# Performance work log

Measured on AMD Instinct MI355X. Metric: run time of the kernel, lower is better.

Reference implementation:

```python
import jax, jax.numpy as jnp
import numpy as np

TOP_K = 2

def setup_inputs() -> dict:
    key = jax.random.key(0)
    k0, k1, k2, k3 = jax.random.split(key, 4)
    B, T, D, F, E = 2, 2048, 1024, 4096, 8
    x = jax.random.normal(k0, (B, T, D), dtype=jnp.float32)
    Wr = jax.random.normal(k1, (E, D), dtype=jnp.float32) * 0.02   # router weight [out=E, in=D]
    W1 = jax.random.normal(k2, (E, F, D), dtype=jnp.float32) * 0.02  # per-expert up-proj [out=F, in=D]
    W2 = jax.random.normal(k3, (E, D, F), dtype=jnp.float32) * 0.02  # per-expert down-proj [out=D, in=F]
    return {"x": x, "Wr": Wr, "W1": W1, "W2": W2}

def reference(x, Wr, W1, W2):
    B, T, D = x.shape
    E = Wr.shape[0]
    N = B * T
    xf = x.reshape(N, D)
    # Router in fp32 on the un-cast activations (as in the torch module).
    logits = xf @ Wr.T                                   # [N, E]
    probs = jax.nn.softmax(logits, axis=-1)
    topk_w, topk_idx = jax.lax.top_k(probs, TOP_K)       # [N, K]
    topk_w = topk_w / jnp.sum(topk_w, axis=-1, keepdims=True)
    # Combine weights scattered into a dense [N, E] dispatch/combine matrix
    # (top_k indices are distinct, so .set is exact).
    combine = jnp.zeros((N, E), dtype=jnp.float32)
    combine = combine.at[jnp.arange(N)[:, None], topk_idx].set(topk_w)
    # Expert FFN runs in bf16 (comm_dtype in the original all-to-all pipeline).
    xb = xf.astype(jnp.bfloat16)
    h = jax.nn.gelu(jnp.einsum('nd,efd->enf', xb, W1.astype(jnp.bfloat16)),
                    approximate=False)                   # [E, N, F]
    yo = jnp.einsum('enf,edf->end', h, W2.astype(jnp.bfloat16))  # [E, N, D]
    # Weighted combine: bf16 expert outputs * fp32 gate weights -> fp32 (torch promotion).
    out = jnp.einsum('end,ne->nd', yo.astype(jnp.float32), combine)
    return out.reshape(B, T, D)
```

## Files before the change

kernel.cpp:

```cpp
#include <hip/hip_runtime.h>
#include <hip/hip_bf16.h>

typedef __attribute__((ext_vector_type(8))) __bf16 bf16x8;
typedef __attribute__((ext_vector_type(4))) float floatx4;

constexpr int N_TOK = 4096;
constexpr int DDIM  = 1024;
constexpr int FDIM  = 4096;
constexpr int NEXP  = 8;
constexpr int NSLOT = 2 * N_TOK;
constexpr int BM_T  = 256;
constexpr int MAXT  = NSLOT / BM_T + NEXP - 1;
constexpr int KSPLIT = 2;

static __device__ __forceinline__ unsigned short f2bf(float f) {
    union { __hip_bfloat16 h; unsigned short u; } v;
    v.h = __float2bfloat16(f);
    return v.u;
}

static __device__ __forceinline__ void gl2lds16(const unsigned short* g, unsigned short* l) {
    __builtin_amdgcn_global_load_lds(
        (__attribute__((address_space(1))) void*)g,
        (__attribute__((address_space(3))) void*)l,
        16, 0, 0);
}

__global__ void castW_kernel(const float* __restrict__ W1, const float* __restrict__ W2,
                             unsigned short* __restrict__ w1b, unsigned short* __restrict__ w2b,
                             int* __restrict__ counts) {
    constexpr int HALF = NEXP * FDIM * DDIM / 4;
    int i = blockIdx.x * 256 + threadIdx.x;
    const float* s; unsigned short* d; int j;
    if (i < HALF) { s = W1; d = w1b; j = i; }
    else          { s = W2; d = w2b; j = i - HALF; }
    float4 v = *(const float4*)(s + (size_t)j * 4);
    ushort4 o;
    o.x = f2bf(v.x); o.y = f2bf(v.y); o.z = f2bf(v.z); o.w = f2bf(v.w);
    *(ushort4*)(d + (size_t)j * 4) = o;
    if (blockIdx.x == 0 && threadIdx.x < NEXP) counts[threadIdx.x] = 0;
}

__global__ void router_kernel(const float* __restrict__ x, const float* __restrict__ Wr,
                              unsigned short* __restrict__ xb,
                              int* __restrict__ te, float* __restrict__ tw,
                              int* __restrict__ counts) {
    __shared__ float wr[NEXP * DDIM];
    const int tid = threadIdx.x;
    for (int i = tid; i < NEXP * DDIM; i += 256) wr[i] = Wr[i];
    __syncthreads();
    const int wave = tid >> 6, lane = tid & 63;
    const int t = blockIdx.x * 4 + wave;

    float xr[16];
    const float* xp = x + (size_t)t * DDIM;
    #pragma unroll
    for (int i = 0; i < 16; i++) xr[i] = xp[lane + 64 * i];

    unsigned short* xbp = xb + (size_t)t * DDIM;
    #pragma unroll
    for (int i = 0; i < 16; i++) xbp[lane + 64 * i] = f2bf(xr[i]);

    float logit[NEXP];
    #pragma unroll
    for (int e = 0; e < NEXP; e++) {
        float s = 0.f;
        #pragma unroll
        for (int i = 0; i < 16; i++) s += xr[i] * wr[e * DDIM + lane + 64 * i];
        #pragma unroll
        for (int off = 32; off > 0; off >>= 1) s += __shfl_xor(s, off, 64);
        logit[e] = s;
    }
    if (lane == 0) {
        int i0 = 0; float l0 = logit[0];
        #pragma unroll
        for (int e = 1; e < NEXP; e++) if (logit[e] > l0) { l0 = logit[e]; i0 = e; }
        int i1 = -1; float l1 = -3.0e38f;
        #pragma unroll
        for (int e = 0; e < NEXP; e++) if (e != i0 && logit[e] > l1) { l1 = logit[e]; i1 = e; }
        float p1 = expf(l1 - l0);
        float w0 = 1.f / (1.f + p1);
        float w1 = p1 * w0;
        te[t * 2] = i0; te[t * 2 + 1] = i1;
        tw[t * 2] = w0; tw[t * 2 + 1] = w1;
        atomicAdd(&counts[i0], 1);
        atomicAdd(&counts[i1], 1);
    }
}

__global__ void scan_scatter_kernel(const int* __restrict__ counts,
                                    const int* __restrict__ te, const float* __restrict__ tw,
                                    int* __restrict__ offsets, int* __restrict__ tile_em,
                                    int* __restrict__ ntile,
                                    int* __restrict__ rowid, float* __restrict__ gate,
                                    int* __restrict__ tok2slot) {
    __shared__ int soff[NEXP];
    __shared__ int scur[NEXP];
    const int tid = threadIdx.x;
    if (tid == 0) {
        int acc = 0, nt = 0;
        for (int e = 0; e < NEXP; e++) {
            offsets[e] = acc; soff[e] = acc;
            for (int m0 = 0; m0 < counts[e]; m0 += BM_T)
                tile_em[nt++] = (e << 16) | (m0 >> 8);
            acc += counts[e];
        }
        offsets[NEXP] = acc;
        ntile[0] = nt;
        for (int i = nt; i < MAXT; i++) tile_em[i] = 0;
    }
    if (tid < NEXP) scur[tid] = 0;
    __syncthreads();
    for (int t = tid; t < N_TOK; t += 256) {
        #pragma unroll
        for (int k = 0; k < 2; k++) {
            int e = te[t * 2 + k];
            int pos = atomicAdd(&scur[e], 1);
            int slot = soff[e] + pos;
            rowid[slot] = t;
            gate[slot] = tw[t * 2 + k];
            tok2slot[t * 2 + k] = slot;
        }
    }
}

template <bool UP>
__global__ __launch_bounds__(512, 4)
void ffn_gemm(const unsigned short* __restrict__ A,
              const unsigned short* __restrict__ Wb,
              unsigned short* __restrict__ Hout,
              float* __restrict__ Y,
              const int* __restrict__ rowid,
              const float* __restrict__ gate,
              const int* __restrict__ offsets,
              const int* __restrict__ tile_em,
              const int* __restrict__ ntile) {
    constexpr int BM = 256, BN = 128, BK = 32;
    constexpr int NOUT = UP ? FDIM : DDIM;
    constexpr int KDIM = UP ? DDIM : FDIM;
    constexpr int NN   = NOUT / BN;
    constexpr int KLEN = UP ? DDIM : (FDIM / KSPLIT);
    constexpr int KT   = KLEN / BK;
    constexpr int MREP = 4, NREP = 4;
    constexpr int ASTRIDE = BM * BK;
    constexpr int BSTRIDE = BN * BK;

    const int nwg = NN * MAXT * (UP ? 1 : KSPLIT);
    const int orig = blockIdx.x;
    const int xcd = orig & 7, idx = orig >> 3;
    const int qq = nwg >> 3, rr8 = nwg & 7;
    const int id = (xcd < rr8 ? xcd * (qq + 1) : rr8 * (qq + 1) + (xcd - rr8) * qq) + idx;

    const int n0 = (id % NN) * BN;
    const int bt = (id / NN) % MAXT;
    const int ks = UP ? 0 : (id / (NN * MAXT));
    if (bt >= ntile[0]) return;
    const int em = tile_em[bt];
    const int e  = em >> 16;
    const int m0 = (em & 0xffff) << 8;
    const int seg = offsets[e];
    const int cnt = offsets[e + 1] - seg;
    const int kbase = ks * KLEN;

    __shared__ __align__(16) unsigned short As[2 * ASTRIDE];
    __shared__ __align__(16) unsigned short Bs[2 * BSTRIDE];

    const int tid  = threadIdx.x;
    const int lane = tid & 63;
    const int wave = tid >> 6;
    const int lrow = lane >> 2;
    const int chunk = lane & 3;
    const int scol = (chunk ^ (lrow & 3)) * 8;

    const unsigned short* ag[2];
    #pragma unroll
    for (int j = 0; j < 2; j++) {
        int arow = wave * 32 + j * 16 + lrow;
        int slot = seg + m0 + arow;
        if (slot >= NSLOT) slot = NSLOT - 1;
        if (UP) { int t = rowid[slot]; ag[j] = A + (size_t)t * DDIM + kbase + scol; }
        else    { ag[j] = A + (size_t)slot * FDIM + kbase + scol; }
    }
    const unsigned short* bg0 =
        Wb + ((size_t)e * NOUT + n0 + wave * 16 + lrow) * KDIM + kbase + scol;

    unsigned short* asl[2];
    #pragma unroll
    for (int j = 0; j < 2; j++)
        asl[j] = &As[(wave * 32 + j * 16) * BK] + lane * 8;
    unsigned short* bsl0 = &Bs[(wave * 16) * BK] + lane * 8;

    auto stage = [&](int b) {
        gl2lds16(ag[0], asl[0] + b * ASTRIDE); ag[0] += BK;
        gl2lds16(ag[1], asl[1] + b * ASTRIDE); ag[1] += BK;
        gl2lds16(bg0,   bsl0   + b * BSTRIDE); bg0   += BK;
    };

    const int frow = lane & 15;
    const int quad = lane >> 4;
    const int wm = (wave >> 1) * 64;
    const int wn = (wave & 1) * 64;
    const int cs = ((quad ^ (frow & 3)) * 8);

    floatx4 acc[MREP][NREP];
    #pragma unroll
    for (int i = 0; i < MREP; i++)
        #pragma unroll
        for (int j = 0; j < NREP; j++)
            acc[i][j] = (floatx4){0.f, 0.f, 0.f, 0.f};

    stage(0);
    __syncthreads();
    for (int kt = 0; kt < KT; kt++) {
        if (kt + 1 < KT) stage((kt + 1) & 1);
        const unsigned short* Ab = &As[(kt & 1) * ASTRIDE];
        const unsigned short* Bb = &Bs[(kt & 1) * BSTRIDE];
        bf16x8 av[MREP], bv[NREP];
        #pragma unroll
        for (int i = 0; i < MREP; i++)
            av[i] = *(const bf16x8*)&Ab[(wm + i * 16 + frow) * BK + cs];
        #pragma unroll
        for (int j = 0; j < NREP; j++)
            bv[j] = *(const bf16x8*)&Bb[(wn + j * 16 + frow) * BK + cs];
        #pragma unroll
        for (int i = 0; i < MREP; i++)
            #pragma unroll
            for (int j = 0; j < NREP; j++)
                acc[i][j] = __builtin_amdgcn_mfma_f32_16x16x32_bf16(av[i], bv[j], acc[i][j], 0, 0, 0);
        __syncthreads();
    }

    #pragma unroll
    for (int mt = 0; mt < MREP; mt++) {
        #pragma unroll
        for (int rg = 0; rg < 4; rg++) {
            int mloc = m0 + wm + mt * 16 + quad * 4 + rg;
            if (mloc >= cnt) continue;
            int slot = seg + mloc;
            if (UP) {
                #pragma unroll
                for (int nt = 0; nt < NREP; nt++) {
                    int n = n0 + wn + nt * 16 + frow;
                    float v = acc[mt][nt][rg];
                    float g = 0.5f * v * (1.0f + erff(v * 0.70710678118654752f));
                    Hout[(size_t)slot * FDIM + n] = f2bf(g);
                }
            } else {
                float gw = gate[slot];
                #pragma unroll
                for (int nt = 0; nt < NREP; nt++) {
                    int n = n0 + wn + nt * 16 + frow;
                    Y[((size_t)ks * NSLOT + slot) * DDIM + n] = gw * acc[mt][nt][rg];
                }
            }
        }
    }
}

__global__ void combine_kernel(const float* __restrict__ Y, const int* __restrict__ tok2slot,
                               float* __restrict__ out) {
    int idx = blockIdx.x * 256 + threadIdx.x;
    int t = idx >> 8;
    int c = (idx & 255) * 4;
    int s0 = tok2slot[t * 2], s1 = tok2slot[t * 2 + 1];
    float4 r = make_float4(0.f, 0.f, 0.f, 0.f);
    #pragma unroll
    for (int ks = 0; ks < KSPLIT; ks++) {
        float4 a = *(const float4*)(Y + ((size_t)ks * NSLOT + s0) * DDIM + c);
        float4 b = *(const float4*)(Y + ((size_t)ks * NSLOT + s1) * DDIM + c);
        r.x += a.x + b.x; r.y += a.y + b.y; r.z += a.z + b.z; r.w += a.w + b.w;
    }
    *(float4*)(out + (size_t)t * DDIM + c) = r;
}

extern "C" void kernel_launch(void* const* d_in, const int* in_sizes, int n_in,
                              void* d_out, int out_size, void* d_ws, size_t ws_size,
                              hipStream_t stream) {
    const float* x  = (const float*)d_in[0];
    const float* Wr = (const float*)d_in[1];
    const float* W1 = (const float*)d_in[2];
    const float* W2 = (const float*)d_in[3];
    float* out = (float*)d_out;

    char* ws = (char*)d_ws;
    size_t off = 0;
    auto alloc = [&](size_t bytes) -> char* {
        char* p = ws + off;
        off = (off + bytes + 255) & ~(size_t)255;
        return p;
    };
    unsigned short* xb   = (unsigned short*)alloc((size_t)N_TOK * DDIM * 2);
    unsigned short* H    = (unsigned short*)alloc((size_t)NSLOT * FDIM * 2);
    float* Yb      = (float*)alloc((size_t)KSPLIT * NSLOT * DDIM * 4);
    int*   rowid   = (int*)alloc(NSLOT * 4);
    float* gatew   = (float*)alloc(NSLOT * 4);
    int*   te      = (int*)alloc(NSLOT * 4);
    float* tw      = (float*)alloc(NSLOT * 4);
    int*   t2s     = (int*)alloc(NSLOT * 4);
    int*   counts  = (int*)alloc(64);
    int*   offsets = (int*)alloc(64);
    int*   tile_em = (int*)alloc(MAXT * 4);
    int*   ntile   = (int*)alloc(64);
    unsigned short* w1b = (unsigned short*)alloc((size_t)NEXP * FDIM * DDIM * 2);
    unsigned short* w2b = (unsigned short*)alloc((size_t)NEXP * DDIM * FDIM * 2);
    (void)ws_size;

    constexpr int GRID_UP = (FDIM / 128) * MAXT;
    constexpr int GRID_DN = (DDIM / 128) * MAXT * KSPLIT;

    castW_kernel<<<2 * NEXP * FDIM * DDIM / 4 / 256, 256, 0, stream>>>(W1, W2, w1b, w2b, counts);
    router_kernel<<<N_TOK / 4, 256, 0, stream>>>(x, Wr, xb, te, tw, counts);
    scan_scatter_kernel<<<1, 256, 0, stream>>>(counts, te, tw, offsets, tile_em, ntile,
                                               rowid, gatew, t2s);
    ffn_gemm<true ><<<GRID_UP, 512, 0, stream>>>(xb, w1b, H, Yb, rowid, gatew,
                                                 offsets, tile_em, ntile);
    ffn_gemm<false><<<GRID_DN, 512, 0, stream>>>(H, w2b, H, Yb, rowid, gatew,
                                                 offsets, tile_em, ntile);
    combine_kernel<<<N_TOK, 256, 0, stream>>>(Yb, t2s, out);
}
```

Baseline: 683.9 us.

## Shrink GEMM tiles to 128x128 with 256 threads and triple-buffered LDS pipeline

Changes the expert FFN GEMMs from 256x128 tiles with 512 threads to 128x128 tiles with 256 threads. This halves the per-tile row granularity, which cuts padding waste on each expert's last tile and produces more workgroups. The K loop moves to a three-stage LDS ring with explicit vmcnt waits and raw barriers, so two loads stay in flight, and MFMA sections get raised wave priority. The LDS swizzle also changes to reduce bank conflicts. In exchange there is less reuse per tile, more B-weight traffic per output, and hand-written waitcnt logic that could be fragile.

Result: faster. 664.3 us (-2.9%).

```diff
diff --git a/kernel.cpp b/kernel.cpp
--- a/kernel.cpp
+++ b/kernel.cpp
@@ -9,7 +9,7 @@
 constexpr int FDIM  = 4096;
 constexpr int NEXP  = 8;
 constexpr int NSLOT = 2 * N_TOK;
-constexpr int BM_T  = 256;
+constexpr int BM_T  = 128;
 constexpr int MAXT  = NSLOT / BM_T + NEXP - 1;
 constexpr int KSPLIT = 2;
 
@@ -102,7 +102,7 @@
         for (int e = 0; e < NEXP; e++) {
             offsets[e] = acc; soff[e] = acc;
             for (int m0 = 0; m0 < counts[e]; m0 += BM_T)
-                tile_em[nt++] = (e << 16) | (m0 >> 8);
+                tile_em[nt++] = (e << 16) | (m0 >> 7);
             acc += counts[e];
         }
         offsets[NEXP] = acc;
@@ -125,7 +125,7 @@
 }
 
 template <bool UP>
-__global__ __launch_bounds__(512, 4)
+__global__ __launch_bounds__(256, 3)
 void ffn_gemm(const unsigned short* __restrict__ A,
               const unsigned short* __restrict__ Wb,
               unsigned short* __restrict__ Hout,
@@ -135,7 +135,7 @@
               const int* __restrict__ offsets,
               const int* __restrict__ tile_em,
               const int* __restrict__ ntile) {
-    constexpr int BM = 256, BN = 128, BK = 32;
+    constexpr int BM = 128, BN = 128, BK = 32;
     constexpr int NOUT = UP ? FDIM : DDIM;
     constexpr int KDIM = UP ? DDIM : FDIM;
     constexpr int NN   = NOUT / BN;
@@ -157,20 +157,20 @@
     if (bt >= ntile[0]) return;
     const int em = tile_em[bt];
     const int e  = em >> 16;
-    const int m0 = (em & 0xffff) << 8;
+    const int m0 = (em & 0xffff) << 7;
     const int seg = offsets[e];
     const int cnt = offsets[e + 1] - seg;
     const int kbase = ks * KLEN;
 
-    __shared__ __align__(16) unsigned short As[2 * ASTRIDE];
-    __shared__ __align__(16) unsigned short Bs[2 * BSTRIDE];
+    __shared__ __align__(16) unsigned short As[3 * ASTRIDE];
+    __shared__ __align__(16) unsigned short Bs[3 * BSTRIDE];
 
     const int tid  = threadIdx.x;
     const int lane = tid & 63;
     const int wave = tid >> 6;
     const int lrow = lane >> 2;
     const int chunk = lane & 3;
-    const int scol = (chunk ^ (lrow & 3)) * 8;
+    const int scol = (chunk ^ ((lrow >> 1) & 3)) * 8;
 
     const unsigned short* ag[2];
     #pragma unroll
@@ -181,26 +181,32 @@
         if (UP) { int t = rowid[slot]; ag[j] = A + (size_t)t * DDIM + kbase + scol; }
         else    { ag[j] = A + (size_t)slot * FDIM + kbase + scol; }
     }
-    const unsigned short* bg0 =
-        Wb + ((size_t)e * NOUT + n0 + wave * 16 + lrow) * KDIM + kbase + scol;
-
+    const unsigned short* bg[2];
+    #pragma unroll
+    for (int j = 0; j < 2; j++) {
+        int brow = wave * 32 + j * 16 + lrow;
+        bg[j] = Wb + ((size_t)e * NOUT + n0 + brow) * KDIM + kbase + scol;
+    }
     unsigned short* asl[2];
-    #pragma unroll
-    for (int j = 0; j < 2; j++)
+    unsigned short* bsl[2];
+    #pragma unroll
+    for (int j = 0; j < 2; j++) {
         asl[j] = &As[(wave * 32 + j * 16) * BK] + lane * 8;
-    unsigned short* bsl0 = &Bs[(wave * 16) * BK] + lane * 8;
+        bsl[j] = &Bs[(wave * 32 + j * 16) * BK] + lane * 8;
+    }
 
     auto stage = [&](int b) {
         gl2lds16(ag[0], asl[0] + b * ASTRIDE); ag[0] += BK;
         gl2lds16(ag[1], asl[1] + b * ASTRIDE); ag[1] += BK;
-        gl2lds16(bg0,   bsl0   + b * BSTRIDE); bg0   += BK;
+        gl2lds16(bg[0], bsl[0] + b * BSTRIDE); bg[0] += BK;
+        gl2lds16(bg[1], bsl[1] + b * BSTRIDE); bg[1] += BK;
     };
 
     const int frow = lane & 15;
     const int quad = lane >> 4;
     const int wm = (wave >> 1) * 64;
     const int wn = (wave & 1) * 64;
-    const int cs = ((quad ^ (frow & 3)) * 8);
+    const int cs = (quad ^ ((frow >> 1) & 3)) * 8;
 
     floatx4 acc[MREP][NREP];
     #pragma unroll
@@ -210,11 +216,17 @@
             acc[i][j] = (floatx4){0.f, 0.f, 0.f, 0.f};
 
     stage(0);
-    __syncthreads();
-    for (int kt = 0; kt < KT; kt++) {
-        if (kt + 1 < KT) stage((kt + 1) & 1);
-        const unsigned short* Ab = &As[(kt & 1) * ASTRIDE];
-        const unsigned short* Bb = &Bs[(kt & 1) * BSTRIDE];
+    stage(1);
+    asm volatile("s_waitcnt vmcnt(4)" ::: "memory");
+    __builtin_amdgcn_s_barrier();
+    __builtin_amdgcn_sched_barrier(0);
+
+    int bc = 0, bs = 2;
+    for (int t = 0; t < KT; ++t) {
+        const bool more = (t + 2 < KT);
+        if (more) stage(bs);
+        const unsigned short* Ab = &As[bc * ASTRIDE];
+        const unsigned short* Bb = &Bs[bc * BSTRIDE];
         bf16x8 av[MREP], bv[NREP];
         #pragma unroll
         for (int i = 0; i < MREP; i++)
@@ -222,12 +234,21 @@
         #pragma unroll
         for (int j = 0; j < NREP; j++)
             bv[j] = *(const bf16x8*)&Bb[(wn + j * 16 + frow) * BK + cs];
+        __builtin_amdgcn_s_setprio(1);
         #pragma unroll
         for (int i = 0; i < MREP; i++)
             #pragma unroll
             for (int j = 0; j < NREP; j++)
                 acc[i][j] = __builtin_amdgcn_mfma_f32_16x16x32_bf16(av[i], bv[j], acc[i][j], 0, 0, 0);
-        __syncthreads();
+        __builtin_amdgcn_s_setprio(0);
+        if (more) asm volatile("s_waitcnt vmcnt(4) lgkmcnt(0)" ::: "memory");
+        else      asm volatile("s_waitcnt vmcnt(0) lgkmcnt(0)" ::: "memory");
+        if (t < KT - 1) {
+            __builtin_amdgcn_s_barrier();
+            __builtin_amdgcn_sched_barrier(0);
+        }
+        bc = (bc == 2) ? 0 : bc + 1;
+        bs = (bs == 2) ? 0 : bs + 1;
     }
 
     #pragma unroll
@@ -312,9 +333,9 @@
     router_kernel<<<N_TOK / 4, 256, 0, stream>>>(x, Wr, xb, te, tw, counts);
     scan_scatter_kernel<<<1, 256, 0, stream>>>(counts, te, tw, offsets, tile_em, ntile,
                                                rowid, gatew, t2s);
-    ffn_gemm<true ><<<GRID_UP, 512, 0, stream>>>(xb, w1b, H, Yb, rowid, gatew,
+    ffn_gemm<true ><<<GRID_UP, 256, 0, stream>>>(xb, w1b, H, Yb, rowid, gatew,
                                                  offsets, tile_em, ntile);
-    ffn_gemm<false><<<GRID_DN, 512, 0, stream>>>(H, w2b, H, Yb, rowid, gatew,
+    ffn_gemm<false><<<GRID_DN, 256, 0, stream>>>(H, w2b, H, Yb, rowid, gatew,
                                                  offsets, tile_em, ntile);
     combine_kernel<<<N_TOK, 256, 0, stream>>>(Yb, t2s, out);
 }
```
